# Kernel optimization log

Measured on AMD Instinct MI355X. Metric: run time of the kernel, lower is better.

The kernel has to match this reference:

```python
import jax, jax.numpy as jnp
import numpy as np

HEADS = 8


def setup_inputs() -> dict:
    key = jax.random.key(0)
    ks = jax.random.split(key, 9)
    B, C, H, W = 16, 512, 32, 32
    d = C // HEADS
    scale = d ** -0.5
    return {
        "x": jax.random.normal(ks[0], (B, C, H, W), dtype=jnp.float32),
        "Wq": jax.random.normal(ks[1], (C, C), dtype=jnp.float32) * (C ** -0.5),
        "bq": jax.random.normal(ks[2], (C,), dtype=jnp.float32) * 0.02,
        "Wk": jax.random.normal(ks[3], (C, C), dtype=jnp.float32) * (C ** -0.5),
        "bk": jax.random.normal(ks[4], (C,), dtype=jnp.float32) * 0.02,
        "Wv": jax.random.normal(ks[5], (C, C), dtype=jnp.float32) * (C ** -0.5),
        "bv": jax.random.normal(ks[6], (C,), dtype=jnp.float32) * 0.02,
        "rel_h": jax.random.normal(ks[7], (d, H, 1), dtype=jnp.float32) * scale,
        "rel_w": jax.random.normal(ks[8], (d, 1, W), dtype=jnp.float32) * scale,
    }


def reference(x, Wq, bq, Wk, bk, Wv, bv, rel_h, rel_w):
    B, C, H, W = x.shape
    heads = HEADS
    d = C // heads
    scale = d ** -0.5
    N = H * W
    xf = x.reshape(B, C, N)  # 1x1 conv == per-pixel linear over channels
    q = (jnp.einsum('oc,bcn->bon', Wq, xf) + bq[:, None]).reshape(B, heads, d, N)
    k = (jnp.einsum('oc,bcn->bon', Wk, xf) + bk[:, None]).reshape(B, heads, d, N)
    v = (jnp.einsum('oc,bcn->bon', Wv, xf) + bv[:, None]).reshape(B, heads, d, N)
    q = q * scale
    # content-content scores [B, heads, N, N]
    cc = jnp.einsum('bhdi,bhdj->bhij', q, k)
    # relative position bias table [d, N], projected by q
    cp_tab = (rel_h + rel_w).reshape(d, N)
    cp = jnp.einsum('bhdi,dj->bhij', q, cp_tab)
    beta = jax.nn.softmax(cc + cp, axis=-1)
    attn = jnp.einsum('bhij,bhdj->bhid', beta, v)  # [B, heads, N, d]
    # original does .view(x.shape) on [b,h,i,d] -> keep same raw reshape
    return attn.reshape(B, C, H, W)
```

## Files before the change

### kernel.cpp

```cpp
#include <hip/hip_runtime.h>
#include <hip/hip_bf16.h>
#include <stdint.h>

typedef unsigned short u16;
typedef u16 u16x8 __attribute__((ext_vector_type(8)));
typedef u16 u16x4 __attribute__((ext_vector_type(4)));
typedef __bf16 bf16x8 __attribute__((ext_vector_type(8)));
typedef float f32x4 __attribute__((ext_vector_type(4)));

#define MFMA16(a, b, c) __builtin_amdgcn_mfma_f32_16x16x32_bf16((a), (b), (c), 0, 0, 0)

#define SCALE_Q 0.18033688011112042f

__device__ __forceinline__ u16 f2b(float f) {
    union { float f; unsigned u; } v; v.f = f;
    unsigned r = v.u + 0x7FFFu + ((v.u >> 16) & 1u);
    return (u16)(r >> 16);
}
__device__ __forceinline__ u16 f2b_h(float f) {
    union { float f; unsigned u; } v; v.f = f;
    return (u16)((v.u + 0x8000u) >> 16);
}

__global__ __launch_bounds__(256) void prep(
    const float* __restrict__ x,
    const float* __restrict__ Wq, const float* __restrict__ Wk,
    const float* __restrict__ Wv,
    u16* __restrict__ wb, u16* __restrict__ xT) {
    __shared__ __align__(16) u16 Ls[128 * 72];
    const int tid = threadIdx.x;

    if (blockIdx.x < 384) {
        int g = blockIdx.x * 256 + tid;
        int which = g >> 15;
        const float* src = which == 0 ? Wq : (which == 1 ? Wk : Wv);
        int off = (g & 32767) * 8;
        f32x4 a = *(const f32x4*)(src + off);
        f32x4 b = *(const f32x4*)(src + off + 4);
        u16x8 o;
#pragma unroll
        for (int i = 0; i < 4; ++i) { o[i] = f2b_h(a[i]); o[4 + i] = f2b_h(b[i]); }
        *(u16x8*)(wb + (size_t)g * 8) = o;
        return;
    }

    const int bid = blockIdx.x - 384;
    const int b  = bid >> 6;
    const int ct = (bid >> 3) & 7;
    const int nt = bid & 7;
    const int C0 = ct * 64, N0 = nt * 128;
    const float* xb = x + ((size_t)b << 19);

#pragma unroll
    for (int rep = 0; rep < 4; ++rep) {
        int id = tid + rep * 256;
        int oct = id >> 7, n = id & 127;
        const float* xp = xb + (size_t)(C0 + oct * 8) * 1024 + N0 + n;
        u16x8 xv;
#pragma unroll
        for (int k = 0; k < 8; ++k) xv[k] = f2b_h(xp[k * 1024]);
        *(u16x8*)(Ls + n * 72 + oct * 8) = xv;
    }
    __syncthreads();
#pragma unroll
    for (int rep = 0; rep < 4; ++rep) {
        int id = tid + rep * 256;
        int n = id >> 3, c8 = id & 7;
        *(u16x8*)(xT + ((size_t)b << 19) + (size_t)(N0 + n) * 512 + C0 + c8 * 8) =
            *(u16x8*)(Ls + n * 72 + c8 * 8);
    }
}

__global__ __launch_bounds__(256, 3) void qkv_proj(
    const u16* __restrict__ xT, const u16* __restrict__ wb,
    const float* __restrict__ bq, const float* __restrict__ bk,
    const float* __restrict__ bv,
    const float* __restrict__ rel_h, const float* __restrict__ rel_w,
    u16* __restrict__ qws, u16* __restrict__ kws, u16* __restrict__ vws) {
    __shared__ __align__(16) u16 Xs[128 * 72];
    __shared__ __align__(16) u16 Ws[128 * 72];

    const int tid  = threadIdx.x;
    const int wave = tid >> 6, lane = tid & 63;
    const int quad = lane >> 4, l16 = lane & 15;
    const int wr = wave >> 1, wc = wave & 1;

    const int id = blockIdx.x;
    const int nt = id & 7;
    const int r  = id >> 3;
    const int o0 = r & 3;
    const int r2 = r >> 2;
    const int mm = r2 % 3;
    const int b  = r2 / 3;
    const int N0 = nt * 128;
    const int O0 = o0 * 128;

    const u16*   W    = wb + (size_t)mm * 262144;
    const float* bias = mm == 0 ? bq : (mm == 1 ? bk : bv);
    const u16*   Xb   = xT + ((size_t)b << 19);

    const int sr = tid >> 3, sc8 = tid & 7;

    u16x8 xr[4], wrg[4];
#pragma unroll
    for (int rp = 0; rp < 4; ++rp) {
        xr[rp]  = *(const u16x8*)(Xb + (size_t)(N0 + sr + rp * 32) * 512 + sc8 * 8);
        wrg[rp] = *(const u16x8*)(W  + (size_t)(O0 + sr + rp * 32) * 512 + sc8 * 8);
    }

    f32x4 acc[4][4] = {};

    for (int kt = 0; kt < 8; ++kt) {
        __syncthreads();
#pragma unroll
        for (int rp = 0; rp < 4; ++rp) {
            *(u16x8*)(Xs + (sr + rp * 32) * 72 + sc8 * 8) = xr[rp];
            *(u16x8*)(Ws + (sr + rp * 32) * 72 + sc8 * 8) = wrg[rp];
        }
        __syncthreads();
        if (kt < 7) {
            int c0 = (kt + 1) * 64;
#pragma unroll
            for (int rp = 0; rp < 4; ++rp) {
                xr[rp]  = *(const u16x8*)(Xb + (size_t)(N0 + sr + rp * 32) * 512 + c0 + sc8 * 8);
                wrg[rp] = *(const u16x8*)(W  + (size_t)(O0 + sr + rp * 32) * 512 + c0 + sc8 * 8);
            }
        }
#pragma unroll
        for (int kk = 0; kk < 2; ++kk) {
            bf16x8 af[4], bfr[4];
#pragma unroll
            for (int mi = 0; mi < 4; ++mi)
                af[mi] = *(bf16x8*)(Xs + (wr * 64 + mi * 16 + l16) * 72 + kk * 32 + quad * 8);
#pragma unroll
            for (int ni = 0; ni < 4; ++ni)
                bfr[ni] = *(bf16x8*)(Ws + (wc * 64 + ni * 16 + l16) * 72 + kk * 32 + quad * 8);
#pragma unroll
            for (int mi = 0; mi < 4; ++mi)
#pragma unroll
                for (int ni = 0; ni < 4; ++ni)
                    acc[mi][ni] = MFMA16(af[mi], bfr[ni], acc[mi][ni]);
        }
    }

#pragma unroll
    for (int mi = 0; mi < 4; ++mi) {
#pragma unroll
        for (int ni = 0; ni < 4; ++ni) {
            int o  = O0 + wc * 64 + ni * 16 + l16;
            int h  = o >> 6, dd = o & 63;
            size_t bh = (size_t)b * 8 + h;
            float bv_ = bias[o];
            int n0 = N0 + wr * 64 + mi * 16 + quad * 4;
            if (mm == 2) {
                u16x4 pk;
#pragma unroll
                for (int rr = 0; rr < 4; ++rr) pk[rr] = f2b(acc[mi][ni][rr] + bv_);
                int qq = (n0 >> 2) & 3, ss = (n0 >> 4) & 1;
                int np = (n0 & ~31) | (qq * 8 + ss * 4);
                *(u16x4*)(vws + (bh * 64 + dd) * 1024 + np) = pk;
            } else if (mm == 0) {
#pragma unroll
                for (int rr = 0; rr < 4; ++rr)
                    qws[(bh * 1024 + (n0 + rr)) * 64 + dd] =
                        f2b((acc[mi][ni][rr] + bv_) * SCALE_Q);
            } else {
                float th = rel_h[dd * 32 + (n0 >> 5)];
                f32x4 tw = *(const f32x4*)(rel_w + dd * 32 + (n0 & 31));
#pragma unroll
                for (int rr = 0; rr < 4; ++rr)
                    kws[(bh * 1024 + n0 + rr) * 64 + dd] =
                        f2b(acc[mi][ni][rr] + bv_ + th + tw[rr]);
            }
        }
    }
}

__global__ __launch_bounds__(256, 4) void attn(
    const u16* __restrict__ qws, const u16* __restrict__ kws,
    const u16* __restrict__ vws, float* __restrict__ out) {
    __shared__ __align__(16) u16 KPb[2][64 * 72];
    __shared__ __align__(16) u16 Vtb[2][64 * 72];

    const int tid  = threadIdx.x;
    const int wave = tid >> 6, lane = tid & 63;
    const int quad = lane >> 4, l16 = lane & 15;
    const int id = blockIdx.x;
    const int h  = id & 7;
    const int qt = (id >> 3) & 7;
    const int b  = id >> 6;
    const size_t bh = (size_t)b * 8 + h;

    const u16* Q = qws + (bh * 1024 + (size_t)qt * 128) * 64;
    const u16* K = kws + bh * 1024 * 64;
    const u16* V = vws + bh * 64 * 1024;

    const int srow = tid >> 3, sc8 = tid & 7;

    bf16x8 qf[2][2];
#pragma unroll
    for (int ni = 0; ni < 2; ++ni)
#pragma unroll
        for (int ks = 0; ks < 2; ++ks)
            qf[ni][ks] = *(const bf16x8*)(Q + (wave * 32 + ni * 16 + l16) * 64 + ks * 32 + quad * 8);

    f32x4 accO[4][2] = {};
    f32x4 s4[2] = {};

    u16x8 kr0, kr1, vr0, vr1;
    kr0 = *(const u16x8*)(K + (size_t)srow * 64 + sc8 * 8);
    kr1 = *(const u16x8*)(K + (size_t)(srow + 32) * 64 + sc8 * 8);
    vr0 = *(const u16x8*)(V + ((size_t)srow << 10) + sc8 * 8);
    vr1 = *(const u16x8*)(V + ((size_t)(srow + 32) << 10) + sc8 * 8);

    for (int jt = 0; jt < 16; ++jt) {
        u16* KP = KPb[jt & 1];
        u16* Vt = Vtb[jt & 1];
        *(u16x8*)(KP + srow * 72 + sc8 * 8)        = kr0;
        *(u16x8*)(KP + (srow + 32) * 72 + sc8 * 8) = kr1;
        *(u16x8*)(Vt + srow * 72 + sc8 * 8)        = vr0;
        *(u16x8*)(Vt + (srow + 32) * 72 + sc8 * 8) = vr1;
        __syncthreads();

        if (jt < 15) {
            const u16* Kn = K + (size_t)(jt + 1) * 64 * 64;
            const u16* Vn = V + (size_t)(jt + 1) * 64;
            kr0 = *(const u16x8*)(Kn + (size_t)srow * 64 + sc8 * 8);
            kr1 = *(const u16x8*)(Kn + (size_t)(srow + 32) * 64 + sc8 * 8);
            vr0 = *(const u16x8*)(Vn + ((size_t)srow << 10) + sc8 * 8);
            vr1 = *(const u16x8*)(Vn + ((size_t)(srow + 32) << 10) + sc8 * 8);
        }

        f32x4 accST[4][2] = {};
#pragma unroll
        for (int ks = 0; ks < 2; ++ks) {
            bf16x8 kf[4];
#pragma unroll
            for (int mj = 0; mj < 4; ++mj)
                kf[mj] = *(bf16x8*)(KP + (mj * 16 + l16) * 72 + ks * 32 + quad * 8);
            __builtin_amdgcn_s_setprio(1);
#pragma unroll
            for (int mj = 0; mj < 4; ++mj)
#pragma unroll
                for (int ni = 0; ni < 2; ++ni)
                    accST[mj][ni] = MFMA16(kf[mj], qf[ni][ks], accST[mj][ni]);
            __builtin_amdgcn_s_setprio(0);
        }

#pragma unroll
        for (int mj = 0; mj < 4; ++mj)
#pragma unroll
            for (int ni = 0; ni < 2; ++ni) {
                f32x4 p;
#pragma unroll
                for (int rr = 0; rr < 4; ++rr)
                    p[rr] = __builtin_amdgcn_exp2f(accST[mj][ni][rr]);
                s4[ni] += p;
                accST[mj][ni] = p;
            }

        union pkun { u16x8 u; bf16x8 b; } pfr[2][2];
#pragma unroll
        for (int ks2 = 0; ks2 < 2; ++ks2)
#pragma unroll
            for (int ni = 0; ni < 2; ++ni) {
                u16x8 t;
#pragma unroll
                for (int rr = 0; rr < 4; ++rr) {
                    t[rr]     = f2b_h(accST[2 * ks2][ni][rr]);
                    t[4 + rr] = f2b_h(accST[2 * ks2 + 1][ni][rr]);
                }
                pfr[ks2][ni].u = t;
            }

#pragma unroll
        for (int ks2 = 0; ks2 < 2; ++ks2) {
            bf16x8 vf[4];
#pragma unroll
            for (int md = 0; md < 4; ++md)
                vf[md] = *(bf16x8*)(Vt + (md * 16 + l16) * 72 + ks2 * 32 + quad * 8);
            __builtin_amdgcn_s_setprio(1);
#pragma unroll
            for (int md = 0; md < 4; ++md)
#pragma unroll
                for (int ni = 0; ni < 2; ++ni)
                    accO[md][ni] = MFMA16(vf[md], pfr[ks2][ni].b, accO[md][ni]);
            __builtin_amdgcn_s_setprio(0);
        }
    }

#pragma unroll
    for (int ni = 0; ni < 2; ++ni) {
        float rs = (s4[ni][0] + s4[ni][1]) + (s4[ni][2] + s4[ni][3]);
        rs += __shfl_xor(rs, 16);
        rs += __shfl_xor(rs, 32);
        float inv = 1.0f / rs;
        int i = qt * 128 + wave * 32 + ni * 16 + l16;
#pragma unroll
        for (int md = 0; md < 4; ++md) {
            f32x4 pk;
#pragma unroll
            for (int rr = 0; rr < 4; ++rr) pk[rr] = accO[md][ni][rr] * inv;
            int dd = md * 16 + quad * 4;
            *(f32x4*)(out + (bh * 1024 + i) * 64 + dd) = pk;
        }
    }
}

extern "C" void kernel_launch(void* const* d_in, const int* in_sizes, int n_in,
                              void* d_out, int out_size, void* d_ws, size_t ws_size,
                              hipStream_t stream) {
    const float* x  = (const float*)d_in[0];
    const float* Wq = (const float*)d_in[1];
    const float* bq = (const float*)d_in[2];
    const float* Wk = (const float*)d_in[3];
    const float* bk = (const float*)d_in[4];
    const float* Wv = (const float*)d_in[5];
    const float* bv = (const float*)d_in[6];
    const float* rh = (const float*)d_in[7];
    const float* rw = (const float*)d_in[8];
    float* out = (float*)d_out;

    u16* kws = (u16*)d_ws;
    u16* vws = kws + 8388608;
    u16* qws = vws + 8388608;
    u16* wb  = qws + 8388608;
    u16* xT  = (u16*)d_out;

    prep<<<1408, 256, 0, stream>>>(x, Wq, Wk, Wv, wb, xT);
    qkv_proj<<<1536, 256, 0, stream>>>(xT, wb, bq, bk, bv, rh, rw, qws, kws, vws);
    attn<<<1024, 256, 0, stream>>>(qws, kws, vws, out);
}
```

Baseline: 204.3 us.

## Load K/V tiles directly to LDS with XOR swizzle and 8 waves per block

Result: slower. 322.3 us (+57.8%).

```diff
diff --git a/kernel.cpp b/kernel.cpp
--- a/kernel.cpp
+++ b/kernel.cpp
@@ -20,6 +20,12 @@
 __device__ __forceinline__ u16 f2b_h(float f) {
     union { float f; unsigned u; } v; v.f = f;
     return (u16)((v.u + 0x8000u) >> 16);
+}
+
+__device__ __forceinline__ void gload16(const u16* g, u16* l) {
+    __builtin_amdgcn_global_load_lds(
+        (const __attribute__((address_space(1))) unsigned int*)g,
+        (__attribute__((address_space(3))) unsigned int*)l, 16, 0, 0);
 }
 
 __global__ __launch_bounds__(256) void prep(
@@ -158,7 +164,9 @@
                 for (int rr = 0; rr < 4; ++rr) pk[rr] = f2b(acc[mi][ni][rr] + bv_);
                 int qq = (n0 >> 2) & 3, ss = (n0 >> 4) & 1;
                 int np = (n0 & ~31) | (qq * 8 + ss * 4);
-                *(u16x4*)(vws + (bh * 64 + dd) * 1024 + np) = pk;
+                int slot = ((np >> 3) & 7) ^ (dd & 7);
+                int np2 = (np & ~63) | (slot << 3) | (np & 7);
+                *(u16x4*)(vws + (bh * 64 + dd) * 1024 + np2) = pk;
             } else if (mm == 0) {
 #pragma unroll
                 for (int rr = 0; rr < 4; ++rr)
@@ -168,19 +176,22 @@
                 float th = rel_h[dd * 32 + (n0 >> 5)];
                 f32x4 tw = *(const f32x4*)(rel_w + dd * 32 + (n0 & 31));
 #pragma unroll
-                for (int rr = 0; rr < 4; ++rr)
-                    kws[(bh * 1024 + n0 + rr) * 64 + dd] =
+                for (int rr = 0; rr < 4; ++rr) {
+                    int n = n0 + rr;
+                    int sdd = (((dd >> 3) ^ (n & 7)) << 3) | (dd & 7);
+                    kws[(bh * 1024 + n) * 64 + sdd] =
                         f2b(acc[mi][ni][rr] + bv_ + th + tw[rr]);
+                }
             }
         }
     }
 }
 
-__global__ __launch_bounds__(256, 4) void attn(
+__global__ __launch_bounds__(512, 8) void attn(
     const u16* __restrict__ qws, const u16* __restrict__ kws,
     const u16* __restrict__ vws, float* __restrict__ out) {
-    __shared__ __align__(16) u16 KPb[2][64 * 72];
-    __shared__ __align__(16) u16 Vtb[2][64 * 72];
+    __shared__ __align__(16) u16 KPb[2][64 * 64];
+    __shared__ __align__(16) u16 Vtb[2][64 * 64];
 
     const int tid  = threadIdx.x;
     const int wave = tid >> 6, lane = tid & 63;
@@ -192,118 +203,106 @@
     const size_t bh = (size_t)b * 8 + h;
 
     const u16* Q = qws + (bh * 1024 + (size_t)qt * 128) * 64;
-    const u16* K = kws + bh * 1024 * 64;
-    const u16* V = vws + bh * 64 * 1024;
-
-    const int srow = tid >> 3, sc8 = tid & 7;
-
-    bf16x8 qf[2][2];
-#pragma unroll
-    for (int ni = 0; ni < 2; ++ni)
-#pragma unroll
-        for (int ks = 0; ks < 2; ++ks)
-            qf[ni][ks] = *(const bf16x8*)(Q + (wave * 32 + ni * 16 + l16) * 64 + ks * 32 + quad * 8);
-
-    f32x4 accO[4][2] = {};
-    f32x4 s4[2] = {};
-
-    u16x8 kr0, kr1, vr0, vr1;
-    kr0 = *(const u16x8*)(K + (size_t)srow * 64 + sc8 * 8);
-    kr1 = *(const u16x8*)(K + (size_t)(srow + 32) * 64 + sc8 * 8);
-    vr0 = *(const u16x8*)(V + ((size_t)srow << 10) + sc8 * 8);
-    vr1 = *(const u16x8*)(V + ((size_t)(srow + 32) << 10) + sc8 * 8);
-
-    for (int jt = 0; jt < 16; ++jt) {
-        u16* KP = KPb[jt & 1];
-        u16* Vt = Vtb[jt & 1];
-        *(u16x8*)(KP + srow * 72 + sc8 * 8)        = kr0;
-        *(u16x8*)(KP + (srow + 32) * 72 + sc8 * 8) = kr1;
-        *(u16x8*)(Vt + srow * 72 + sc8 * 8)        = vr0;
-        *(u16x8*)(Vt + (srow + 32) * 72 + sc8 * 8) = vr1;
+    const u16* K = kws + bh * 65536;
+    const u16* V = vws + bh * 65536;
+
+    const int lrow = wave * 8 + (lane >> 3);
+    const int lc8  = lane & 7;
+    const u16* Kl = K + (size_t)lrow * 64 + lc8 * 8;
+    const u16* Vl = V + ((size_t)lrow << 10) + lc8 * 8;
+    u16* const KP0 = &KPb[0][0];
+    u16* const Vt0 = &Vtb[0][0];
+    const int wofs = wave * 512;
+
+    bf16x8 qf[2];
+#pragma unroll
+    for (int ks = 0; ks < 2; ++ks)
+        qf[ks] = *(const bf16x8*)(Q + (wave * 16 + l16) * 64 + ks * 32 + quad * 8);
+
+    const int xsw = (l16 & 7) << 4;
+    const int xk0 = (quad * 16) ^ xsw;
+    const int xk1 = (64 + quad * 16) ^ xsw;
+
+    f32x4 accO[4] = {};
+    f32x4 s4 = {};
+
+    gload16(Kl, KP0 + wofs);
+    gload16(Vl, Vt0 + wofs);
+
+    auto body = [&](int jt, int cur) {
         __syncthreads();
-
         if (jt < 15) {
-            const u16* Kn = K + (size_t)(jt + 1) * 64 * 64;
-            const u16* Vn = V + (size_t)(jt + 1) * 64;
-            kr0 = *(const u16x8*)(Kn + (size_t)srow * 64 + sc8 * 8);
-            kr1 = *(const u16x8*)(Kn + (size_t)(srow + 32) * 64 + sc8 * 8);
-            vr0 = *(const u16x8*)(Vn + ((size_t)srow << 10) + sc8 * 8);
-            vr1 = *(const u16x8*)(Vn + ((size_t)(srow + 32) << 10) + sc8 * 8);
-        }
-
-        f32x4 accST[4][2] = {};
+            int nxt = cur ^ 1;
+            gload16(Kl + (jt + 1) * 4096, KP0 + nxt * 4096 + wofs);
+            gload16(Vl + (jt + 1) * 64,  Vt0 + nxt * 4096 + wofs);
+        }
+        const char* KP = (const char*)(KP0 + cur * 4096);
+        const char* Vt = (const char*)(Vt0 + cur * 4096);
+
+        f32x4 accST[4] = {};
 #pragma unroll
         for (int ks = 0; ks < 2; ++ks) {
+            const int xo = ks ? xk1 : xk0;
             bf16x8 kf[4];
 #pragma unroll
             for (int mj = 0; mj < 4; ++mj)
-                kf[mj] = *(bf16x8*)(KP + (mj * 16 + l16) * 72 + ks * 32 + quad * 8);
+                kf[mj] = *(const bf16x8*)(KP + (mj * 16 + l16) * 128 + xo);
             __builtin_amdgcn_s_setprio(1);
 #pragma unroll
             for (int mj = 0; mj < 4; ++mj)
-#pragma unroll
-                for (int ni = 0; ni < 2; ++ni)
-                    accST[mj][ni] = MFMA16(kf[mj], qf[ni][ks], accST[mj][ni]);
+                accST[mj] = MFMA16(kf[mj], qf[ks], accST[mj]);
             __builtin_amdgcn_s_setprio(0);
         }
 
 #pragma unroll
-        for (int mj = 0; mj < 4; ++mj)
-#pragma unroll
-            for (int ni = 0; ni < 2; ++ni) {
-                f32x4 p;
-#pragma unroll
-                for (int rr = 0; rr < 4; ++rr)
-                    p[rr] = __builtin_amdgcn_exp2f(accST[mj][ni][rr]);
-                s4[ni] += p;
-                accST[mj][ni] = p;
+        for (int mj = 0; mj < 4; ++mj) {
+            f32x4 p;
+#pragma unroll
+            for (int rr = 0; rr < 4; ++rr)
+                p[rr] = __builtin_amdgcn_exp2f(accST[mj][rr]);
+            s4 += p;
+            accST[mj] = p;
+        }
+
+#pragma unroll
+        for (int ks2 = 0; ks2 < 2; ++ks2) {
+            union { u16x8 u; bf16x8 b; } pfr;
+            u16x8 t;
+#pragma unroll
+            for (int rr = 0; rr < 4; ++rr) {
+                t[rr]     = f2b_h(accST[2 * ks2][rr]);
+                t[4 + rr] = f2b_h(accST[2 * ks2 + 1][rr]);
             }
-
-        union pkun { u16x8 u; bf16x8 b; } pfr[2][2];
-#pragma unroll
-        for (int ks2 = 0; ks2 < 2; ++ks2)
-#pragma unroll
-            for (int ni = 0; ni < 2; ++ni) {
-                u16x8 t;
-#pragma unroll
-                for (int rr = 0; rr < 4; ++rr) {
-                    t[rr]     = f2b_h(accST[2 * ks2][ni][rr]);
-                    t[4 + rr] = f2b_h(accST[2 * ks2 + 1][ni][rr]);
-                }
-                pfr[ks2][ni].u = t;
-            }
-
-#pragma unroll
-        for (int ks2 = 0; ks2 < 2; ++ks2) {
+            pfr.u = t;
+            const int xo = ks2 ? xk1 : xk0;
             bf16x8 vf[4];
 #pragma unroll
             for (int md = 0; md < 4; ++md)
-                vf[md] = *(bf16x8*)(Vt + (md * 16 + l16) * 72 + ks2 * 32 + quad * 8);
+                vf[md] = *(const bf16x8*)(Vt + (md * 16 + l16) * 128 + xo);
             __builtin_amdgcn_s_setprio(1);
 #pragma unroll
             for (int md = 0; md < 4; ++md)
-#pragma unroll
-                for (int ni = 0; ni < 2; ++ni)
-                    accO[md][ni] = MFMA16(vf[md], pfr[ks2][ni].b, accO[md][ni]);
+                accO[md] = MFMA16(vf[md], pfr.b, accO[md]);
             __builtin_amdgcn_s_setprio(0);
         }
-    }
-
-#pragma unroll
-    for (int ni = 0; ni < 2; ++ni) {
-        float rs = (s4[ni][0] + s4[ni][1]) + (s4[ni][2] + s4[ni][3]);
-        rs += __shfl_xor(rs, 16);
-        rs += __shfl_xor(rs, 32);
-        float inv = 1.0f / rs;
-        int i = qt * 128 + wave * 32 + ni * 16 + l16;
-#pragma unroll
-        for (int md = 0; md < 4; ++md) {
-            f32x4 pk;
-#pragma unroll
-            for (int rr = 0; rr < 4; ++rr) pk[rr] = accO[md][ni][rr] * inv;
-            int dd = md * 16 + quad * 4;
-            *(f32x4*)(out + (bh * 1024 + i) * 64 + dd) = pk;
-        }
+    };
+
+    for (int j2 = 0; j2 < 8; ++j2) {
+        body(2 * j2,     0);
+        body(2 * j2 + 1, 1);
+    }
+
+    float rs = (s4[0] + s4[1]) + (s4[2] + s4[3]);
+    rs += __shfl_xor(rs, 16);
+    rs += __shfl_xor(rs, 32);
+    float inv = 1.0f / rs;
+    int i = qt * 128 + wave * 16 + l16;
+#pragma unroll
+    for (int md = 0; md < 4; ++md) {
+        f32x4 pk;
+#pragma unroll
+        for (int rr = 0; rr < 4; ++rr) pk[rr] = accO[md][rr] * inv;
+        *(f32x4*)(out + (bh * 1024 + i) * 64 + md * 16 + quad * 4) = pk;
     }
 }
 
@@ -329,5 +328,5 @@
 
     prep<<<1408, 256, 0, stream>>>(x, Wq, Wk, Wv, wb, xT);
     qkv_proj<<<1536, 256, 0, stream>>>(xT, wb, bq, bk, bv, rh, rw, qws, kws, vws);
-    attn<<<1024, 256, 0, stream>>>(qws, kws, vws, out);
-}
+    attn<<<1024, 512, 0, stream>>>(qws, kws, vws, out);
+}
```
